# Kernel optimization log

Hardware: AMD Instinct MI355X
Metric: run time of the kernel (lower is better)

The kernel has to match this reference:

```python
import jax, jax.numpy as jnp
import numpy as np

NEG_SLOPE = 0.1
BN_EPS = 1e-5

def lrelu(z):
    return jax.nn.leaky_relu(z, NEG_SLOPE)

def conv1d(x, w, b):
    # x: [B,C,L], w: [O,I,K], 'same' padding for K=3
    y = jax.lax.conv_general_dilated(x, w, (1,), [(1, 1)], dimension_numbers=('NCH', 'OIH', 'NCH'))
    return y + b[None, :, None]

def batchnorm_train(x, g, be):
    # training-mode BatchNorm1d over (B, L) per channel; x: [B,C,L]
    m = x.mean(axis=(0, 2), keepdims=True)
    v = x.var(axis=(0, 2), keepdims=True)
    return g[None, :, None] * (x - m) * jax.lax.rsqrt(v + BN_EPS) + be[None, :, None]

def setup_inputs() -> dict:
    key = jax.random.key(0)
    ks = jax.random.split(key, 16)
    L, B, E = 100, 32, 512
    F, K, M, H, DEC = 256, 3, 128, 512, 512
    D = F + 2  # cnn feats + 2 coord dims
    s = 0.02
    inp = {
        'x': jax.random.normal(ks[0], (L, B, E), jnp.float32),
        'h': jax.random.normal(ks[1], (B, H), jnp.float32),
        'cw1': jax.random.normal(ks[2], (F, E, K), jnp.float32) * s,
        'cb1': jnp.zeros((F,), jnp.float32),
        'g1': jnp.ones((F,), jnp.float32), 'be1': jnp.zeros((F,), jnp.float32),
        'cw2': jax.random.normal(ks[3], (F, F, K), jnp.float32) * s,
        'cb2': jnp.zeros((F,), jnp.float32),
        'g2': jnp.ones((F,), jnp.float32), 'be2': jnp.zeros((F,), jnp.float32),
        'cw3': jax.random.normal(ks[4], (F, F, K), jnp.float32) * s,
        'cb3': jnp.zeros((F,), jnp.float32),
        'g3': jnp.ones((F,), jnp.float32), 'be3': jnp.zeros((F,), jnp.float32),
        'cw4': jax.random.normal(ks[5], (F, F, K), jnp.float32) * s,
        'cb4': jnp.zeros((F,), jnp.float32),
        'g4': jnp.ones((F,), jnp.float32), 'be4': jnp.zeros((F,), jnp.float32),
        'W1': jax.random.normal(ks[6], (2 * D + H, M), jnp.float32) * s,
        'b1': jnp.zeros((M,), jnp.float32),
        'W2': jax.random.normal(ks[7], (M, M), jnp.float32) * s,
        'b2': jnp.zeros((M,), jnp.float32),
        'W3': jax.random.normal(ks[8], (M, M), jnp.float32) * s,
        'b3': jnp.zeros((M,), jnp.float32),
        'W4': jax.random.normal(ks[9], (M, M), jnp.float32) * s,
        'b4': jnp.zeros((M,), jnp.float32),
        'F1': jax.random.normal(ks[10], (M, M), jnp.float32) * s,
        'fb1': jnp.zeros((M,), jnp.float32),
        'F2': jax.random.normal(ks[11], (M, DEC), jnp.float32) * s,
        'fb2': jnp.zeros((DEC,), jnp.float32),
    }
    return inp

def reference(x, h, cw1, cb1, g1, be1, cw2, cb2, g2, be2, cw3, cb3, g3, be3,
              cw4, cb4, g4, be4, W1, b1, W2, b2, W3, b3, W4, b4, F1, fb1, F2, fb2):
    # x: [L,B,E] -> [B,E,L]
    xc = jnp.transpose(x, (1, 2, 0))
    for cw, cb, g, be in ((cw1, cb1, g1, be1), (cw2, cb2, g2, be2),
                          (cw3, cb3, g3, be3), (cw4, cb4, g4, be4)):
        xc = batchnorm_train(lrelu(conv1d(xc, cw, cb)), g, be)
    xc = jnp.transpose(xc, (0, 2, 1))  # [B,L,F]
    B, L, _ = xc.shape
    # coordinate tensor: cvt_coord(i, L) = [(i/sqrt(L)-2)/2, (i%sqrt(L)-2)/2]
    i = jnp.arange(L, dtype=jnp.float32)
    sL = jnp.sqrt(jnp.float32(L))
    coord = jnp.stack([(i / sL - 2.0) / 2.0, (jnp.mod(i, sL) - 2.0) / 2.0], axis=-1)
    xf = jnp.concatenate([xc, jnp.broadcast_to(coord, (B, L, 2))], axis=-1)  # [B,L,D]
    D = xf.shape[-1]
    # pair[b,i,j] = [xf[b,j], xf[b,i], h[b]]; split W1 to avoid materializing concat
    Wa, Wb, Wc = W1[:D], W1[D:2 * D], W1[2 * D:]
    A = xf @ Wa                              # contribution of x_j, [B,L,M]
    C = xf @ Wb + (h @ Wc + b1)[:, None, :]  # contribution of x_i and h, [B,L,M]
    g = lrelu(C[:, :, None, :] + A[:, None, :, :])  # [B,L,L,M]
    g = lrelu(g @ W2 + b2)
    g = lrelu(g @ W3 + b3)
    g = lrelu(g @ W4 + b4)
    s = g.sum(axis=(1, 2))  # sum-pool over all L*L pairs -> [B,M]
    out = lrelu(lrelu(s @ F1 + fb1) @ F2 + fb2)  # [B,dec_hid]
    return out
```

## Files before the change

### kernel.cpp

```cpp
#include <hip/hip_runtime.h>
#include <hip/hip_bf16.h>
#include <stdint.h>
#include <stddef.h>

#define NEG 0.1f

typedef __attribute__((ext_vector_type(8))) short short8;
typedef __attribute__((ext_vector_type(16))) float floatx16;

__device__ __forceinline__ unsigned f2bf(float f) {
  union { float f; unsigned u; } v; v.f = f;
  unsigned r = v.u + 0x7FFFu + ((v.u >> 16) & 1u);
  return r >> 16;
}
__device__ __forceinline__ unsigned pk2bf(float a, float b) {
  __hip_bfloat162 hh = __float22bfloat162_rn(make_float2(a, b));
  union { __hip_bfloat162 h; unsigned u; } v; v.h = hh; return v.u;
}
__device__ __forceinline__ float bits2f(unsigned u) {
  union { unsigned u; float f; } v; v.u = u; return v.f;
}

__global__ void k_prep(const float* __restrict__ cw1, const float* __restrict__ cw2,
                       const float* __restrict__ cw3, const float* __restrict__ cw4,
                       unsigned short* __restrict__ wt1, unsigned short* __restrict__ wt2,
                       unsigned short* __restrict__ wt3, unsigned short* __restrict__ wt4,
                       const float* __restrict__ W1, unsigned short* __restrict__ wab,
                       const float* __restrict__ W2, const float* __restrict__ W3,
                       const float* __restrict__ W4, unsigned short* __restrict__ wmlp,
                       const float* __restrict__ h, float* __restrict__ hc,
                       const float* __restrict__ F1v, const float* __restrict__ F2v,
                       float* __restrict__ wsink) {
  __shared__ float tile[64 * 65];
  int bid = blockIdx.x, tid = threadIdx.x;
  if (bid < 1280) {
    int z = bid;
    int E; const float* cw; unsigned short* wt;
    if (z < 512) { E = 512; cw = cw1; wt = wt1; }
    else {
      int q = (z - 512) >> 8; E = 256;
      cw = (q == 0) ? cw2 : ((q == 1) ? cw3 : cw4);
      wt = (q == 0) ? wt2 : ((q == 1) ? wt3 : wt4);
      z = (z - 512) & 255;
    }
    int idx = z * 256 + tid;
    int f = idx / E, e = idx - f * E;
    const float* s = cw + (size_t)idx * 3;
    unsigned short* d = wt + (size_t)f * 3 * E + e;
    d[0] = (unsigned short)f2bf(s[0]);
    d[E] = (unsigned short)f2bf(s[1]);
    d[2 * E] = (unsigned short)f2bf(s[2]);
  } else if (bid < 1304) {
    int tw = bid - 1280;
    int half = tw / 12, rem = tw % 12, dt = rem >> 1, nt = rem & 1;
    int c = tid & 63, rq = tid >> 6;
#pragma unroll
    for (int it = 0; it < 16; ++it) {
      int r = rq + it * 4;
      int kp = dt * 64 + r;
      float v = 0.f;
      if (kp < 258) v = W1[(size_t)(half * 258 + kp) * 128 + nt * 64 + c];
      tile[r * 65 + c] = v;
    }
    __syncthreads();
#pragma unroll
    for (int it = 0; it < 16; ++it) {
      int r2 = rq + it * 4;
      wab[(size_t)(half * 128 + nt * 64 + r2) * 384 + dt * 64 + c] =
          (unsigned short)f2bf(tile[c * 65 + r2]);
    }
  } else if (bid < 1496) {
    int i2 = (bid - 1304) * 256 + tid;
    int n = i2 & 127, k = (i2 >> 7) & 127, zz = i2 >> 14;
    const float* W = (zz == 0) ? W2 : ((zz == 1) ? W3 : W4);
    float v = W[k * 128 + n];
    int w = n >> 5, l = ((k >> 3) & 1) * 32 + (n & 31), kk = k >> 4, j = k & 7;
    int i = (((zz * 4 + w) * 8 + kk) << 9) | (l << 3) | j;
    wmlp[i] = (unsigned short)f2bf(v);
  } else {
    int t = bid - 1496;
    int b = t >> 2, seg = t & 3;
    int m = tid & 127, sub = tid >> 7;
    int k0 = seg * 128 + sub * 64;
    const float* hr = h + b * 512 + k0;
    const float* Wc = W1 + (size_t)(516 + k0) * 128 + m;
    float a0 = 0.f, a1 = 0.f, a2 = 0.f, a3 = 0.f, a4 = 0.f, a5 = 0.f, a6 = 0.f, a7 = 0.f;
#pragma unroll
    for (int k = 0; k < 64; k += 8) {
      a0 += hr[k + 0] * Wc[(size_t)(k + 0) * 128];
      a1 += hr[k + 1] * Wc[(size_t)(k + 1) * 128];
      a2 += hr[k + 2] * Wc[(size_t)(k + 2) * 128];
      a3 += hr[k + 3] * Wc[(size_t)(k + 3) * 128];
      a4 += hr[k + 4] * Wc[(size_t)(k + 4) * 128];
      a5 += hr[k + 5] * Wc[(size_t)(k + 5) * 128];
      a6 += hr[k + 6] * Wc[(size_t)(k + 6) * 128];
      a7 += hr[k + 7] * Wc[(size_t)(k + 7) * 128];
    }
    float s = ((a0 + a1) + (a2 + a3)) + ((a4 + a5) + (a6 + a7));
    atomicAdd(&hc[b * 128 + m], s);
  }
  {
    int wslice = bid % 80;
    const float* wsrc = (wslice < 64) ? (F2v + (size_t)wslice * 1024)
                                      : (F1v + (size_t)(wslice - 64) * 1024);
    float4 v = *(const float4*)(wsrc + tid * 4);
    float sv = v.x + v.y + v.z + v.w;
    if (sv == 1234.5678f) wsink[0] = sv;
  }
}

__global__ __launch_bounds__(128, 2) void k_conv(
    const float* __restrict__ zin, const float* __restrict__ bnin,
    const float* __restrict__ gamv, const float* __restrict__ betv,
    const unsigned short* __restrict__ wt, const float* __restrict__ cb,
    float* __restrict__ zout, float* __restrict__ bnout, int E, int xmode) {
  extern __shared__ unsigned short smem[];
  const int SL = (E == 512) ? 520 : 264;
  unsigned short* slab = smem;
  unsigned short* Bs = smem + 34 * SL;
  const int K = 3 * E, NC = K >> 6, NCH = NC >> 1;
  const int esh = (E == 512) ? 9 : 8;
  int tid = threadIdx.x;
  int lane = tid & 63, khalf = tid >> 6;
  int r0 = blockIdx.x * 32, ct = blockIdx.y;
  int i32 = lane & 31;
  int koff = (lane >> 5) << 3;

  int lrow = (r0 + i32) % 100;
  bool vks0 = (lrow >= 1), vks2 = (lrow <= 98);

  if (xmode) {
    for (int s = khalf; s < 34; s += 2) {
      int m = r0 - 1 + s; m = min(max(m, 0), 3199);
      int b = m / 100, l = m - b * 100;
      size_t base = (size_t)(l * 32 + b) * 512;
#pragma unroll
      for (int cc = 0; cc < 2; ++cc) {
        int ch = cc * 256 + lane * 4;
        float4 v = *(const float4*)(zin + base + ch);
        uint2 p; p.x = pk2bf(v.x, v.y); p.y = pk2bf(v.z, v.w);
        *(uint2*)(&slab[s * SL + ch]) = p;
      }
    }
  } else {
    const float inv = 1.f / 3200.f;
    float sc[4], sh[4];
#pragma unroll
    for (int q = 0; q < 4; ++q) {
      int ch = lane * 4 + q;
      float mme = bnin[ch] * inv;
      float var = bnin[256 + ch] * inv - mme * mme;
      sc[q] = gamv[ch] * rsqrtf(var + 1e-5f);
      sh[q] = betv[ch] - mme * sc[q];
    }
    for (int s = khalf; s < 34; s += 2) {
      int m = r0 - 1 + s; m = min(max(m, 0), 3199);
      float4 v = *(const float4*)(zin + (size_t)m * 256 + lane * 4);
      uint2 p;
      p.x = pk2bf(v.x * sc[0] + sh[0], v.y * sc[1] + sh[1]);
      p.y = pk2bf(v.z * sc[2] + sh[2], v.w * sc[3] + sh[3]);
      *(uint2*)(&slab[s * SL + lane * 4]) = p;
    }
  }
  __syncthreads();

  floatx16 acc;
#pragma unroll
  for (int q = 0; q < 16; ++q) acc[q] = 0.f;

  unsigned short* Bc = Bs + khalf * (32 * 72);
  int brow = lane >> 1, bseg = (lane & 1) * 32;
  const unsigned short* wrow = wt + (size_t)(ct * 32 + brow) * K + khalf * NCH * 64 + bseg;
  uint4 pre[4];
#pragma unroll
  for (int t = 0; t < 4; ++t) pre[t] = *(const uint4*)(wrow + t * 8);

  for (int c = 0; c < NCH; ++c) {
#pragma unroll
    for (int t = 0; t < 4; ++t)
      *(uint4*)(&Bc[brow * 72 + bseg + t * 8]) = pre[t];
    if (c + 1 < NCH) {
#pragma unroll
      for (int t = 0; t < 4; ++t)
        pre[t] = *(const uint4*)(wrow + (c + 1) * 64 + t * 8);
    }
    int cg = khalf * NCH + c;
    int ks = (cg << 6) >> esh;
    int ebase = (cg << 6) & (E - 1);
    bool v = (ks == 0) ? vks0 : ((ks == 2) ? vks2 : true);
    int srow = i32 + ks;
#pragma unroll
    for (int kk = 0; kk < 4; ++kk) {
      short8 a = {};
      if (v) a = *(const short8*)(&slab[srow * SL + ebase + kk * 16 + koff]);
      short8 b8 = *(const short8*)(&Bc[i32 * 72 + kk * 16 + koff]);
      acc = __builtin_amdgcn_mfma_f32_32x32x16_bf16(a, b8, acc, 0, 0, 0);
    }
  }

  __syncthreads();
  float* scr = (float*)smem;
  if (khalf == 1) {
#pragma unroll
    for (int reg = 0; reg < 16; ++reg) {
      int rowp = (reg & 3) + 8 * (reg >> 2) + 4 * (lane >> 5);
      scr[rowp * 32 + i32] = acc[reg];
    }
  }
  __syncthreads();
  if (khalf == 0) {
    int f = ct * 32 + i32;
    float bias = cb[f];
    float s1 = 0.f, s2 = 0.f;
#pragma unroll
    for (int reg = 0; reg < 16; ++reg) {
      int rowp = (reg & 3) + 8 * (reg >> 2) + 4 * (lane >> 5);
      int m = r0 + rowp;
      float v = acc[reg] + scr[rowp * 32 + i32] + bias;
      v = fmaxf(v, NEG * v);
      zout[(size_t)m * 256 + f] = v;
      s1 += v; s2 += v * v;
    }
    s1 += __shfl_xor(s1, 32, 64);
    s2 += __shfl_xor(s2, 32, 64);
    if (lane < 32) { atomicAdd(&bnout[f], s1); atomicAdd(&bnout[256 + f], s2); }
  }
}

__global__ __launch_bounds__(128, 2) void k_ac(
    const float* __restrict__ zin, const float* __restrict__ bnin,
    const float* __restrict__ gamv, const float* __restrict__ betv,
    const unsigned short* __restrict__ wab, const float* __restrict__ hc,
    const float* __restrict__ b1v,
    unsigned short* __restrict__ Abf, unsigned short* __restrict__ Cbf) {
  __shared__ unsigned short slab[32 * 328];
  __shared__ unsigned short Bs[2 * 64 * 72];
  int tid = threadIdx.x;
  int lane = tid & 63, wave = tid >> 6;
  int r0 = blockIdx.x * 32, ct = blockIdx.y;
  int i32 = lane & 31;
  int koff = (lane >> 5) << 3;
  const float inv = 1.f / 3200.f;

  {
    float sc[4], sh[4];
#pragma unroll
    for (int q = 0; q < 4; ++q) {
      int ch = lane * 4 + q;
      float mme = bnin[ch] * inv;
      float var = bnin[256 + ch] * inv - mme * mme;
      sc[q] = gamv[ch] * rsqrtf(var + 1e-5f);
      sh[q] = betv[ch] - mme * sc[q];
    }
    for (int s = wave; s < 32; s += 2) {
      int m = r0 + s;
      float4 v = *(const float4*)(zin + (size_t)m * 256 + lane * 4);
      uint2 p;
      p.x = pk2bf(v.x * sc[0] + sh[0], v.y * sc[1] + sh[1]);
      p.y = pk2bf(v.z * sc[2] + sh[2], v.w * sc[3] + sh[3]);
      *(uint2*)(&slab[s * 328 + lane * 4]) = p;
    }
    if (wave == 0) {
      int s = i32, half = (lane >> 5) * 32;
      int m = r0 + s, l = m % 100;
      float c0 = ((float)l * 0.1f - 2.0f) * 0.5f;
      float c1 = ((float)(l % 10) - 2.0f) * 0.5f;
#pragma unroll
      for (int seg = 0; seg < 4; ++seg) {
        uint4 z4; z4.x = z4.y = z4.z = z4.w = 0u;
        if (half == 0 && seg == 0) z4.x = pk2bf(c0, c1);
        *(uint4*)(&slab[s * 328 + 256 + half + seg * 8]) = z4;
      }
    }
  }

  floatx16 acc;
#pragma unroll
  for (int q = 0; q < 16; ++q) acc[q] = 0.f;

  int brow = tid >> 1, bhalf = (tid & 1) * 32;
  uint4 pre[4];
#pragma unroll
  for (int t = 0; t < 4; ++t)
    pre[t] = *(const uint4*)(wab + (size_t)(ct * 64 + brow) * 384 + bhalf + t * 8);

  for (int c = 0; c < 5; ++c) {
    unsigned short* Bc = Bs + (c & 1) * (64 * 72);
#pragma unroll
    for (int t = 0; t < 4; ++t)
      *(uint4*)(&Bc[brow * 72 + bhalf + t * 8]) = pre[t];
    __syncthreads();
    if (c + 1 < 5) {
#pragma unroll
      for (int t = 0; t < 4; ++t)
        pre[t] = *(const uint4*)(wab + (size_t)(ct * 64 + brow) * 384 + (c + 1) * 64 + bhalf + t * 8);
    }
#pragma unroll
    for (int kk = 0; kk < 4; ++kk) {
      short8 a = *(const short8*)(&slab[i32 * 328 + c * 64 + kk * 16 + koff]);
      short8 b8 = *(const short8*)(&Bs[(c & 1) * (64 * 72) + (wave * 32 + i32) * 72 + kk * 16 + koff]);
      acc = __builtin_amdgcn_mfma_f32_32x32x16_bf16(a, b8, acc, 0, 0, 0);
    }
  }

  int n = ct * 64 + wave * 32 + i32;
#pragma unroll
  for (int reg = 0; reg < 16; ++reg) {
    int rowp = (reg & 3) + 8 * (reg >> 2) + 4 * (lane >> 5);
    int m = r0 + rowp;
    float v = acc[reg];
    if (ct < 2) {
      Abf[(size_t)m * 128 + n] = (unsigned short)f2bf(v);
    } else {
      int b = m / 100;
      int nc = n - 128;
      Cbf[(size_t)m * 128 + nc] =
          (unsigned short)f2bf(v + hc[b * 128 + nc] + b1v[nc]);
    }
  }
}

__global__ __launch_bounds__(256, 2) void k_mlp(
    const unsigned short* __restrict__ Abf, const unsigned short* __restrict__ Cbf,
    const unsigned short* __restrict__ wmlp, const float* __restrict__ b2,
    const float* __restrict__ b3, const float* __restrict__ b4,
    float* __restrict__ sout) {
  __shared__ unsigned short gs0[128 * 128];
  __shared__ unsigned short gs1[128 * 128];
  int tid = threadIdx.x, lane = tid & 63, wave = tid >> 6;
  int ln31 = lane & 31;
  int half = lane >> 5;
  int rx = ln31 & 15;

  short8 wreg[3][8];
#pragma unroll
  for (int z = 0; z < 3; ++z)
#pragma unroll
    for (int kk = 0; kk < 8; ++kk)
      wreg[z][kk] = *(const short8*)(wmlp + (size_t)(((z * 4 + wave) * 8 + kk) * 512) + lane * 8);

  int wb = wave * 32;
  float4 bq[2][4];
#pragma unroll
  for (int q = 0; q < 4; ++q) {
    bq[0][q] = *(const float4*)(b2 + wb + q * 8 + 4 * half);
    bq[1][q] = *(const float4*)(b3 + wb + q * 8 + 4 * half);
  }
  float bv4 = b4[wb + ln31];

  for (int ti = 0; ti < 2; ++ti) {
    int t = blockIdx.x + ti * 1264;
    int b = t / 79, tt = t - b * 79;
    __syncthreads();
    {
      int lr = wb + (lane >> 1);
      int hh = lane & 1;
      int lbase = lr * 128, lrx = lr & 15;
      int r = tt * 128 + lr;
      if (r > 9999) r = 9999;
      const unsigned short* Crow = Cbf + (size_t)(b * 100 + r / 100) * 128;
      const unsigned short* Arow = Abf + (size_t)(b * 100 + r % 100) * 128;
#pragma unroll
      for (int it = 0; it < 8; ++it) {
        int cc = hh * 64 + it * 8;
        uint4 c4 = *(const uint4*)(Crow + cc);
        uint4 a4 = *(const uint4*)(Arow + cc);
        unsigned cw[4] = {c4.x, c4.y, c4.z, c4.w};
        unsigned aw[4] = {a4.x, a4.y, a4.z, a4.w};
        unsigned ow[4];
#pragma unroll
        for (int q = 0; q < 4; ++q) {
          float x0 = bits2f(cw[q] << 16) + bits2f(aw[q] << 16);
          float x1 = bits2f(cw[q] & 0xFFFF0000u) + bits2f(aw[q] & 0xFFFF0000u);
          x0 = fmaxf(x0, NEG * x0);
          x1 = fmaxf(x1, NEG * x1);
          ow[q] = pk2bf(x0, x1);
        }
        uint4 o4; o4.x = ow[0]; o4.y = ow[1]; o4.z = ow[2]; o4.w = ow[3];
        *(uint4*)(&gs0[lbase + (((hh * 8 + it) ^ lrx) << 3)]) = o4;
      }
    }
    __syncthreads();

#pragma unroll
    for (int z = 0; z < 2; ++z) {
      const unsigned short* src = z ? gs1 : gs0;
      unsigned short* dst = z ? gs0 : gs1;
#pragma unroll
      for (int rg = 0; rg < 4; ++rg) {
        floatx16 acc;
#pragma unroll
        for (int q = 0; q < 16; ++q) acc[q] = 0.f;
        int rowb = (rg * 32 + ln31) * 128;
#pragma unroll
        for (int kk = 0; kk < 8; ++kk) {
          short8 g8 = *(const short8*)(&src[rowb + (((kk * 2 + half) ^ rx) << 3)]);
          acc = __builtin_amdgcn_mfma_f32_32x32x16_bf16(wreg[z][kk], g8, acc, 0, 0, 0);
        }
        int prb = (rg * 32 + ln31) * 128;
#pragma unroll
        for (int q = 0; q < 4; ++q) {
          float4 bb = bq[z][q];
          float v0 = acc[q * 4 + 0] + bb.x; v0 = fmaxf(v0, NEG * v0);
          float v1 = acc[q * 4 + 1] + bb.y; v1 = fmaxf(v1, NEG * v1);
          float v2 = acc[q * 4 + 2] + bb.z; v2 = fmaxf(v2, NEG * v2);
          float v3 = acc[q * 4 + 3] + bb.w; v3 = fmaxf(v3, NEG * v3);
          uint2 p; p.x = pk2bf(v0, v1); p.y = pk2bf(v2, v3);
          *(uint2*)(&dst[prb + (((wave * 4 + q) ^ rx) << 3) + half * 4]) = p;
        }
      }
      __syncthreads();
    }

    float colsum = 0.f;
#pragma unroll
    for (int rg = 0; rg < 4; ++rg) {
      floatx16 acc;
#pragma unroll
      for (int q = 0; q < 16; ++q) acc[q] = 0.f;
      int rowb = (rg * 32 + ln31) * 128;
#pragma unroll
      for (int kk = 0; kk < 8; ++kk) {
        short8 a8 = *(const short8*)(&gs0[rowb + (((kk * 2 + half) ^ rx) << 3)]);
        acc = __builtin_amdgcn_mfma_f32_32x32x16_bf16(a8, wreg[2][kk], acc, 0, 0, 0);
      }
#pragma unroll
      for (int reg = 0; reg < 16; ++reg) {
        int rowp = (reg & 3) + 8 * (reg >> 2) + 4 * half;
        int p = tt * 128 + rg * 32 + rowp;
        float v = acc[reg] + bv4;
        v = fmaxf(v, NEG * v);
        colsum += (p < 10000) ? v : 0.f;
      }
    }
    colsum += __shfl_xor(colsum, 32, 64);
    if (lane < 32) atomicAdd(&sout[b * 128 + wb + lane], colsum);
  }
}

__global__ void k_final(const float* __restrict__ s, const float* __restrict__ F1,
                        const float* __restrict__ fb1, const float* __restrict__ F2,
                        const float* __restrict__ fb2, float* __restrict__ out) {
  __shared__ float sl[128], part[512], t1[128];
  int b = blockIdx.x, t = threadIdx.x;
  if (t < 128) sl[t] = s[b * 128 + t];
  __syncthreads();
  {
    int m = t & 127, kh = t >> 7;
    const float* Fp = F1 + m;
    float a0 = 0.f, a1 = 0.f, a2 = 0.f, a3 = 0.f;
    for (int k = kh * 32; k < kh * 32 + 32; k += 4) {
      a0 += sl[k + 0] * Fp[(size_t)(k + 0) * 128];
      a1 += sl[k + 1] * Fp[(size_t)(k + 1) * 128];
      a2 += sl[k + 2] * Fp[(size_t)(k + 2) * 128];
      a3 += sl[k + 3] * Fp[(size_t)(k + 3) * 128];
    }
    part[t] = (a0 + a1) + (a2 + a3);
  }
  __syncthreads();
  if (t < 128) {
    float a = (part[t] + part[t + 128]) + (part[t + 256] + part[t + 384]) + fb1[t];
    t1[t] = fmaxf(a, NEG * a);
  }
  __syncthreads();
  {
    int o = t;
    const float* Fp = F2 + o;
    float a0 = fb2[o], a1 = 0.f, a2 = 0.f, a3 = 0.f;
    for (int k = 0; k < 128; k += 4) {
      a0 += t1[k + 0] * Fp[(size_t)(k + 0) * 512];
      a1 += t1[k + 1] * Fp[(size_t)(k + 1) * 512];
      a2 += t1[k + 2] * Fp[(size_t)(k + 2) * 512];
      a3 += t1[k + 3] * Fp[(size_t)(k + 3) * 512];
    }
    float a = (a0 + a1) + (a2 + a3);
    out[b * 512 + o] = fmaxf(a, NEG * a);
  }
}

extern "C" void kernel_launch(void* const* d_in, const int* in_sizes, int n_in,
                              void* d_out, int out_size, void* d_ws, size_t ws_size,
                              hipStream_t stream) {
  const float* x   = (const float*)d_in[0];
  const float* h   = (const float*)d_in[1];
  const float* cw1 = (const float*)d_in[2];
  const float* cb1 = (const float*)d_in[3];
  const float* g1  = (const float*)d_in[4];
  const float* be1 = (const float*)d_in[5];
  const float* cw2 = (const float*)d_in[6];
  const float* cb2 = (const float*)d_in[7];
  const float* g2  = (const float*)d_in[8];
  const float* be2 = (const float*)d_in[9];
  const float* cw3 = (const float*)d_in[10];
  const float* cb3 = (const float*)d_in[11];
  const float* g3  = (const float*)d_in[12];
  const float* be3 = (const float*)d_in[13];
  const float* cw4 = (const float*)d_in[14];
  const float* cb4 = (const float*)d_in[15];
  const float* g4  = (const float*)d_in[16];
  const float* be4 = (const float*)d_in[17];
  const float* W1  = (const float*)d_in[18];
  const float* b1  = (const float*)d_in[19];
  const float* W2  = (const float*)d_in[20];
  const float* b2  = (const float*)d_in[21];
  const float* W3  = (const float*)d_in[22];
  const float* b3  = (const float*)d_in[23];
  const float* W4  = (const float*)d_in[24];
  const float* b4  = (const float*)d_in[25];
  const float* F1  = (const float*)d_in[26];
  const float* fb1 = (const float*)d_in[27];
  const float* F2  = (const float*)d_in[28];
  const float* fb2 = (const float*)d_in[29];

  char* ws = (char*)d_ws;
  float* bn0  = (float*)(ws + 0);
  float* bn1  = (float*)(ws + 2048);
  float* bn2  = (float*)(ws + 4096);
  float* bn3  = (float*)(ws + 6144);
  float* sbuf = (float*)(ws + 8192);
  float* hc   = (float*)(ws + 24576);
  float* za   = (float*)(ws + 40960);
  float* zb   = (float*)(ws + 3317760);
  unsigned short* wt1  = (unsigned short*)(ws + 6594560);
  unsigned short* wt2  = (unsigned short*)(ws + 7380992);
  unsigned short* wt3  = (unsigned short*)(ws + 7774208);
  unsigned short* wt4  = (unsigned short*)(ws + 8167424);
  unsigned short* wab  = (unsigned short*)(ws + 8560640);
  unsigned short* wmlp = (unsigned short*)(ws + 8757248);
  unsigned short* Abf  = (unsigned short*)(ws + 8855552);
  unsigned short* Cbf  = (unsigned short*)(ws + 9674752);
  float* wsink = (float*)(ws + 10493952);

  hipMemsetAsync(d_ws, 0, 40960, stream);

  k_prep<<<1624, 256, 0, stream>>>(cw1, cw2, cw3, cw4, wt1, wt2, wt3, wt4,
                                   W1, wab, W2, W3, W4, wmlp, h, hc, F1, F2, wsink);

  const int lds1 = (34 * 520 + 2 * 32 * 72) * 2;
  const int lds2 = (34 * 264 + 2 * 32 * 72) * 2;
  k_conv<<<dim3(100, 8), 128, lds1, stream>>>(x,  nullptr, nullptr, nullptr, wt1, cb1, za, bn0, 512, 1);
  k_conv<<<dim3(100, 8), 128, lds2, stream>>>(za, bn0, g1, be1, wt2, cb2, zb, bn1, 256, 0);
  k_conv<<<dim3(100, 8), 128, lds2, stream>>>(zb, bn1, g2, be2, wt3, cb3, za, bn2, 256, 0);
  k_conv<<<dim3(100, 8), 128, lds2, stream>>>(za, bn2, g3, be3, wt4, cb4, zb, bn3, 256, 0);

  k_ac<<<dim3(100, 4), 128, 0, stream>>>(zb, bn3, g4, be4, wab, hc, b1, Abf, Cbf);

  k_mlp<<<1264, 256, 0, stream>>>(Abf, Cbf, wmlp, b2, b3, b4, sbuf);
  k_final<<<32, 512, 0, stream>>>(sbuf, F1, fb1, F2, fb2, (float*)d_out);
}
```

Measured before the change: 289.8 us.

## Make k_mlp waves own row slabs, single LDS buffer, one tile per block

Reworks the pairwise MLP kernel so each wave processes its own 32 rows through all 128 output columns, which removes the block-wide syncthreads between layers and lets a single in-place LDS buffer replace two. Weights are now streamed from global/L2 per output tile instead of being held in registers. The grid is doubled to one tile per block and launch bounds are raised to 3 blocks per CU to improve occupancy. The trade-off is repeated weight loads from cache and more atomics per block, one per output column tile. A small cleanup in k_ac indexes the B tile through the already computed buffer pointer.

```diff
diff --git a/kernel.cpp b/kernel.cpp
--- a/kernel.cpp
+++ b/kernel.cpp
@@ -298,7 +298,7 @@
 #pragma unroll
     for (int kk = 0; kk < 4; ++kk) {
       short8 a = *(const short8*)(&slab[i32 * 328 + c * 64 + kk * 16 + koff]);
-      short8 b8 = *(const short8*)(&Bs[(c & 1) * (64 * 72) + (wave * 32 + i32) * 72 + kk * 16 + koff]);
+      short8 b8 = *(const short8*)(&Bc[(wave * 32 + i32) * 72 + kk * 16 + koff]);
       acc = __builtin_amdgcn_mfma_f32_32x32x16_bf16(a, b8, acc, 0, 0, 0);
     }
   }
@@ -320,121 +320,116 @@
   }
 }
 
-__global__ __launch_bounds__(256, 2) void k_mlp(
+__global__ __launch_bounds__(256, 3) void k_mlp(
     const unsigned short* __restrict__ Abf, const unsigned short* __restrict__ Cbf,
     const unsigned short* __restrict__ wmlp, const float* __restrict__ b2,
     const float* __restrict__ b3, const float* __restrict__ b4,
     float* __restrict__ sout) {
-  __shared__ unsigned short gs0[128 * 128];
-  __shared__ unsigned short gs1[128 * 128];
+  __shared__ unsigned short gs[128 * 128];
   int tid = threadIdx.x, lane = tid & 63, wave = tid >> 6;
   int ln31 = lane & 31;
   int half = lane >> 5;
   int rx = ln31 & 15;
-
-  short8 wreg[3][8];
-#pragma unroll
-  for (int z = 0; z < 3; ++z)
+  int wb = wave * 32;
+
+  int t = blockIdx.x;
+  int b = t / 79, tt = t - b * 79;
+
+  {
+    int lr = wb + (lane >> 1);
+    int hh = lane & 1;
+    int lbase = lr * 128, lrx = lr & 15;
+    int r = tt * 128 + lr;
+    if (r > 9999) r = 9999;
+    const unsigned short* Crow = Cbf + (size_t)(b * 100 + r / 100) * 128;
+    const unsigned short* Arow = Abf + (size_t)(b * 100 + r % 100) * 128;
+#pragma unroll
+    for (int it = 0; it < 8; ++it) {
+      int cc = hh * 64 + it * 8;
+      uint4 c4 = *(const uint4*)(Crow + cc);
+      uint4 a4 = *(const uint4*)(Arow + cc);
+      unsigned cw[4] = {c4.x, c4.y, c4.z, c4.w};
+      unsigned aw[4] = {a4.x, a4.y, a4.z, a4.w};
+      unsigned ow[4];
+#pragma unroll
+      for (int q = 0; q < 4; ++q) {
+        float x0 = bits2f(cw[q] << 16) + bits2f(aw[q] << 16);
+        float x1 = bits2f(cw[q] & 0xFFFF0000u) + bits2f(aw[q] & 0xFFFF0000u);
+        x0 = fmaxf(x0, NEG * x0);
+        x1 = fmaxf(x1, NEG * x1);
+        ow[q] = pk2bf(x0, x1);
+      }
+      uint4 o4; o4.x = ow[0]; o4.y = ow[1]; o4.z = ow[2]; o4.w = ow[3];
+      *(uint4*)(&gs[lbase + (((hh * 8 + it) ^ lrx) << 3)]) = o4;
+    }
+  }
+
+  int rowb = (wb + ln31) * 128;
+
+#pragma unroll
+  for (int z = 0; z < 2; ++z) {
+    const float* bz = z ? b3 : b2;
+    short8 gfrag[8];
 #pragma unroll
     for (int kk = 0; kk < 8; ++kk)
-      wreg[z][kk] = *(const short8*)(wmlp + (size_t)(((z * 4 + wave) * 8 + kk) * 512) + lane * 8);
-
-  int wb = wave * 32;
-  float4 bq[2][4];
-#pragma unroll
-  for (int q = 0; q < 4; ++q) {
-    bq[0][q] = *(const float4*)(b2 + wb + q * 8 + 4 * half);
-    bq[1][q] = *(const float4*)(b3 + wb + q * 8 + 4 * half);
-  }
-  float bv4 = b4[wb + ln31];
-
-  for (int ti = 0; ti < 2; ++ti) {
-    int t = blockIdx.x + ti * 1264;
-    int b = t / 79, tt = t - b * 79;
-    __syncthreads();
-    {
-      int lr = wb + (lane >> 1);
-      int hh = lane & 1;
-      int lbase = lr * 128, lrx = lr & 15;
-      int r = tt * 128 + lr;
-      if (r > 9999) r = 9999;
-      const unsigned short* Crow = Cbf + (size_t)(b * 100 + r / 100) * 128;
-      const unsigned short* Arow = Abf + (size_t)(b * 100 + r % 100) * 128;
-#pragma unroll
-      for (int it = 0; it < 8; ++it) {
-        int cc = hh * 64 + it * 8;
-        uint4 c4 = *(const uint4*)(Crow + cc);
-        uint4 a4 = *(const uint4*)(Arow + cc);
-        unsigned cw[4] = {c4.x, c4.y, c4.z, c4.w};
-        unsigned aw[4] = {a4.x, a4.y, a4.z, a4.w};
-        unsigned ow[4];
-#pragma unroll
-        for (int q = 0; q < 4; ++q) {
-          float x0 = bits2f(cw[q] << 16) + bits2f(aw[q] << 16);
-          float x1 = bits2f(cw[q] & 0xFFFF0000u) + bits2f(aw[q] & 0xFFFF0000u);
-          x0 = fmaxf(x0, NEG * x0);
-          x1 = fmaxf(x1, NEG * x1);
-          ow[q] = pk2bf(x0, x1);
-        }
-        uint4 o4; o4.x = ow[0]; o4.y = ow[1]; o4.z = ow[2]; o4.w = ow[3];
-        *(uint4*)(&gs0[lbase + (((hh * 8 + it) ^ lrx) << 3)]) = o4;
+      gfrag[kk] = *(const short8*)(&gs[rowb + (((kk * 2 + half) ^ rx) << 3)]);
+#pragma unroll
+    for (int nt = 0; nt < 4; ++nt) {
+      const unsigned short* wp = wmlp + (size_t)(((z * 4 + nt) * 8) << 9) + lane * 8;
+      short8 wfrag[8];
+#pragma unroll
+      for (int kk = 0; kk < 8; ++kk)
+        wfrag[kk] = *(const short8*)(wp + (kk << 9));
+      floatx16 acc;
+#pragma unroll
+      for (int q = 0; q < 16; ++q) acc[q] = 0.f;
+#pragma unroll
+      for (int kk = 0; kk < 8; ++kk)
+        acc = __builtin_amdgcn_mfma_f32_32x32x16_bf16(wfrag[kk], gfrag[kk], acc, 0, 0, 0);
+#pragma unroll
+      for (int q = 0; q < 4; ++q) {
+        float4 bb = *(const float4*)(bz + nt * 32 + q * 8 + 4 * half);
+        float v0 = acc[q * 4 + 0] + bb.x; v0 = fmaxf(v0, NEG * v0);
+        float v1 = acc[q * 4 + 1] + bb.y; v1 = fmaxf(v1, NEG * v1);
+        float v2 = acc[q * 4 + 2] + bb.z; v2 = fmaxf(v2, NEG * v2);
+        float v3 = acc[q * 4 + 3] + bb.w; v3 = fmaxf(v3, NEG * v3);
+        uint2 p; p.x = pk2bf(v0, v1); p.y = pk2bf(v2, v3);
+        *(uint2*)(&gs[rowb + (((nt * 4 + q) ^ rx) << 3) + half * 4]) = p;
       }
     }
-    __syncthreads();
-
-#pragma unroll
-    for (int z = 0; z < 2; ++z) {
-      const unsigned short* src = z ? gs1 : gs0;
-      unsigned short* dst = z ? gs0 : gs1;
-#pragma unroll
-      for (int rg = 0; rg < 4; ++rg) {
-        floatx16 acc;
-#pragma unroll
-        for (int q = 0; q < 16; ++q) acc[q] = 0.f;
-        int rowb = (rg * 32 + ln31) * 128;
-#pragma unroll
-        for (int kk = 0; kk < 8; ++kk) {
-          short8 g8 = *(const short8*)(&src[rowb + (((kk * 2 + half) ^ rx) << 3)]);
-          acc = __builtin_amdgcn_mfma_f32_32x32x16_bf16(wreg[z][kk], g8, acc, 0, 0, 0);
-        }
-        int prb = (rg * 32 + ln31) * 128;
-#pragma unroll
-        for (int q = 0; q < 4; ++q) {
-          float4 bb = bq[z][q];
-          float v0 = acc[q * 4 + 0] + bb.x; v0 = fmaxf(v0, NEG * v0);
-          float v1 = acc[q * 4 + 1] + bb.y; v1 = fmaxf(v1, NEG * v1);
-          float v2 = acc[q * 4 + 2] + bb.z; v2 = fmaxf(v2, NEG * v2);
-          float v3 = acc[q * 4 + 3] + bb.w; v3 = fmaxf(v3, NEG * v3);
-          uint2 p; p.x = pk2bf(v0, v1); p.y = pk2bf(v2, v3);
-          *(uint2*)(&dst[prb + (((wave * 4 + q) ^ rx) << 3) + half * 4]) = p;
-        }
-      }
-      __syncthreads();
-    }
-
-    float colsum = 0.f;
-#pragma unroll
-    for (int rg = 0; rg < 4; ++rg) {
+  }
+
+  {
+    short8 gfrag[8];
+#pragma unroll
+    for (int kk = 0; kk < 8; ++kk)
+      gfrag[kk] = *(const short8*)(&gs[rowb + (((kk * 2 + half) ^ rx) << 3)]);
+#pragma unroll
+    for (int nt = 0; nt < 4; ++nt) {
+      const unsigned short* wp = wmlp + (size_t)(((8 + nt) * 8) << 9) + lane * 8;
+      short8 wfrag[8];
+#pragma unroll
+      for (int kk = 0; kk < 8; ++kk)
+        wfrag[kk] = *(const short8*)(wp + (kk << 9));
       floatx16 acc;
 #pragma unroll
       for (int q = 0; q < 16; ++q) acc[q] = 0.f;
-      int rowb = (rg * 32 + ln31) * 128;
-#pragma unroll
-      for (int kk = 0; kk < 8; ++kk) {
-        short8 a8 = *(const short8*)(&gs0[rowb + (((kk * 2 + half) ^ rx) << 3)]);
-        acc = __builtin_amdgcn_mfma_f32_32x32x16_bf16(a8, wreg[2][kk], acc, 0, 0, 0);
-      }
+#pragma unroll
+      for (int kk = 0; kk < 8; ++kk)
+        acc = __builtin_amdgcn_mfma_f32_32x32x16_bf16(gfrag[kk], wfrag[kk], acc, 0, 0, 0);
+      float bv = b4[nt * 32 + ln31];
+      float cs = 0.f;
 #pragma unroll
       for (int reg = 0; reg < 16; ++reg) {
         int rowp = (reg & 3) + 8 * (reg >> 2) + 4 * half;
-        int p = tt * 128 + rg * 32 + rowp;
-        float v = acc[reg] + bv4;
+        int p = tt * 128 + wb + rowp;
+        float v = acc[reg] + bv;
         v = fmaxf(v, NEG * v);
-        colsum += (p < 10000) ? v : 0.f;
+        cs += (p < 10000) ? v : 0.f;
       }
-    }
-    colsum += __shfl_xor(colsum, 32, 64);
-    if (lane < 32) atomicAdd(&sout[b * 128 + wb + lane], colsum);
+      cs += __shfl_xor(cs, 32, 64);
+      if (lane < 32) atomicAdd(&sout[b * 128 + nt * 32 + lane], cs);
+    }
   }
 }
 
@@ -545,6 +540,6 @@
 
   k_ac<<<dim3(100, 4), 128, 0, stream>>>(zb, bn3, g4, be4, wab, hc, b1, Abf, Cbf);
 
-  k_mlp<<<1264, 256, 0, stream>>>(Abf, Cbf, wmlp, b2, b3, b4, sbuf);
+  k_mlp<<<2528, 256, 0, stream>>>(Abf, Cbf, wmlp, b2, b3, b4, sbuf);
   k_final<<<32, 512, 0, stream>>>(sbuf, F1, fb1, F2, fb2, (float*)d_out);
 }
```

After: 313.3 us. 1.08x slower.

## Widen conv blocks to 64 output channels and vectorize weight prep

Applied to the files above, without the earlier changes.

The conv kernel now runs 256 threads per block, with four waves split as two K-halves by two 32-channel column groups. Each block covers 64 output channels, so the grid halves and every activation slab loaded into LDS is reused across twice as many channels. The B tile becomes double-buffered with a barrier per chunk, replacing the single barrier after the slab load, which adds synchronisation inside the loop. Weight prep also converts four taps per thread with float4 loads and packed bf16 stores, cutting the prep grid from 1624 to 664 blocks.

```diff
diff --git a/kernel.cpp b/kernel.cpp
--- a/kernel.cpp
+++ b/kernel.cpp
@@ -33,25 +33,35 @@
                        float* __restrict__ wsink) {
   __shared__ float tile[64 * 65];
   int bid = blockIdx.x, tid = threadIdx.x;
-  if (bid < 1280) {
-    int z = bid;
-    int E; const float* cw; unsigned short* wt;
-    if (z < 512) { E = 512; cw = cw1; wt = wt1; }
-    else {
-      int q = (z - 512) >> 8; E = 256;
+  if (bid < 320) {
+    const float* cw; unsigned short* wt; int E, base;
+    if (bid < 128) {
+      cw = cw1; wt = wt1; E = 512;
+      base = (bid * 256 + tid) * 4;
+    } else {
+      int j = bid - 128; int q = j >> 6; E = 256;
       cw = (q == 0) ? cw2 : ((q == 1) ? cw3 : cw4);
       wt = (q == 0) ? wt2 : ((q == 1) ? wt3 : wt4);
-      z = (z - 512) & 255;
-    }
-    int idx = z * 256 + tid;
-    int f = idx / E, e = idx - f * E;
-    const float* s = cw + (size_t)idx * 3;
-    unsigned short* d = wt + (size_t)f * 3 * E + e;
-    d[0] = (unsigned short)f2bf(s[0]);
-    d[E] = (unsigned short)f2bf(s[1]);
-    d[2 * E] = (unsigned short)f2bf(s[2]);
-  } else if (bid < 1304) {
-    int tw = bid - 1280;
+      base = (((j & 63) * 256) + tid) * 4;
+    }
+    int f = base / E, e0 = base & (E - 1);
+    const float* s = cw + (size_t)(f * E + e0) * 3;
+    float4 v0 = *(const float4*)(s);
+    float4 v1 = *(const float4*)(s + 4);
+    float4 v2 = *(const float4*)(s + 8);
+    float k0[4] = {v0.x, v0.w, v1.z, v2.y};
+    float k1[4] = {v0.y, v1.x, v1.w, v2.z};
+    float k2[4] = {v0.z, v1.y, v2.x, v2.w};
+    unsigned short* d = wt + (size_t)f * 3 * E + e0;
+    uint2 p;
+    p.x = pk2bf(k0[0], k0[1]); p.y = pk2bf(k0[2], k0[3]);
+    *(uint2*)(d) = p;
+    p.x = pk2bf(k1[0], k1[1]); p.y = pk2bf(k1[2], k1[3]);
+    *(uint2*)(d + E) = p;
+    p.x = pk2bf(k2[0], k2[1]); p.y = pk2bf(k2[2], k2[3]);
+    *(uint2*)(d + 2 * E) = p;
+  } else if (bid < 344) {
+    int tw = bid - 320;
     int half = tw / 12, rem = tw % 12, dt = rem >> 1, nt = rem & 1;
     int c = tid & 63, rq = tid >> 6;
 #pragma unroll
@@ -69,8 +79,8 @@
       wab[(size_t)(half * 128 + nt * 64 + r2) * 384 + dt * 64 + c] =
           (unsigned short)f2bf(tile[c * 65 + r2]);
     }
-  } else if (bid < 1496) {
-    int i2 = (bid - 1304) * 256 + tid;
+  } else if (bid < 536) {
+    int i2 = (bid - 344) * 256 + tid;
     int n = i2 & 127, k = (i2 >> 7) & 127, zz = i2 >> 14;
     const float* W = (zz == 0) ? W2 : ((zz == 1) ? W3 : W4);
     float v = W[k * 128 + n];
@@ -78,7 +88,7 @@
     int i = (((zz * 4 + w) * 8 + kk) << 9) | (l << 3) | j;
     wmlp[i] = (unsigned short)f2bf(v);
   } else {
-    int t = bid - 1496;
+    int t = bid - 536;
     int b = t >> 2, seg = t & 3;
     int m = tid & 127, sub = tid >> 7;
     int k0 = seg * 128 + sub * 64;
@@ -109,7 +119,7 @@
   }
 }
 
-__global__ __launch_bounds__(128, 2) void k_conv(
+__global__ __launch_bounds__(256, 2) void k_conv(
     const float* __restrict__ zin, const float* __restrict__ bnin,
     const float* __restrict__ gamv, const float* __restrict__ betv,
     const unsigned short* __restrict__ wt, const float* __restrict__ cb,
@@ -121,7 +131,8 @@
   const int K = 3 * E, NC = K >> 6, NCH = NC >> 1;
   const int esh = (E == 512) ? 9 : 8;
   int tid = threadIdx.x;
-  int lane = tid & 63, khalf = tid >> 6;
+  int lane = tid & 63, wave = tid >> 6;
+  int khalf = wave >> 1, cwave = wave & 1;
   int r0 = blockIdx.x * 32, ct = blockIdx.y;
   int i32 = lane & 31;
   int koff = (lane >> 5) << 3;
@@ -130,7 +141,7 @@
   bool vks0 = (lrow >= 1), vks2 = (lrow <= 98);
 
   if (xmode) {
-    for (int s = khalf; s < 34; s += 2) {
+    for (int s = wave; s < 34; s += 4) {
       int m = r0 - 1 + s; m = min(max(m, 0), 3199);
       int b = m / 100, l = m - b * 100;
       size_t base = (size_t)(l * 32 + b) * 512;
@@ -153,7 +164,7 @@
       sc[q] = gamv[ch] * rsqrtf(var + 1e-5f);
       sh[q] = betv[ch] - mme * sc[q];
     }
-    for (int s = khalf; s < 34; s += 2) {
+    for (int s = wave; s < 34; s += 4) {
       int m = r0 - 1 + s; m = min(max(m, 0), 3199);
       float4 v = *(const float4*)(zin + (size_t)m * 256 + lane * 4);
       uint2 p;
@@ -162,23 +173,24 @@
       *(uint2*)(&slab[s * SL + lane * 4]) = p;
     }
   }
-  __syncthreads();
 
   floatx16 acc;
 #pragma unroll
   for (int q = 0; q < 16; ++q) acc[q] = 0.f;
 
-  unsigned short* Bc = Bs + khalf * (32 * 72);
-  int brow = lane >> 1, bseg = (lane & 1) * 32;
-  const unsigned short* wrow = wt + (size_t)(ct * 32 + brow) * K + khalf * NCH * 64 + bseg;
+  int t128 = tid & 127;
+  int brow = t128 >> 1, bhalf = (t128 & 1) * 32;
+  const unsigned short* wrow = wt + (size_t)(ct * 64 + brow) * K + khalf * NCH * 64 + bhalf;
   uint4 pre[4];
 #pragma unroll
   for (int t = 0; t < 4; ++t) pre[t] = *(const uint4*)(wrow + t * 8);
 
   for (int c = 0; c < NCH; ++c) {
+    unsigned short* Bc = Bs + (khalf * 2 + (c & 1)) * (64 * 72);
 #pragma unroll
     for (int t = 0; t < 4; ++t)
-      *(uint4*)(&Bc[brow * 72 + bseg + t * 8]) = pre[t];
+      *(uint4*)(&Bc[brow * 72 + bhalf + t * 8]) = pre[t];
+    __syncthreads();
     if (c + 1 < NCH) {
 #pragma unroll
       for (int t = 0; t < 4; ++t)
@@ -193,7 +205,7 @@
     for (int kk = 0; kk < 4; ++kk) {
       short8 a = {};
       if (v) a = *(const short8*)(&slab[srow * SL + ebase + kk * 16 + koff]);
-      short8 b8 = *(const short8*)(&Bc[i32 * 72 + kk * 16 + koff]);
+      short8 b8 = *(const short8*)(&Bc[(cwave * 32 + i32) * 72 + kk * 16 + koff]);
       acc = __builtin_amdgcn_mfma_f32_32x32x16_bf16(a, b8, acc, 0, 0, 0);
     }
   }
@@ -204,19 +216,19 @@
 #pragma unroll
     for (int reg = 0; reg < 16; ++reg) {
       int rowp = (reg & 3) + 8 * (reg >> 2) + 4 * (lane >> 5);
-      scr[rowp * 32 + i32] = acc[reg];
+      scr[cwave * 1024 + rowp * 32 + i32] = acc[reg];
     }
   }
   __syncthreads();
   if (khalf == 0) {
-    int f = ct * 32 + i32;
+    int f = ct * 64 + cwave * 32 + i32;
     float bias = cb[f];
     float s1 = 0.f, s2 = 0.f;
 #pragma unroll
     for (int reg = 0; reg < 16; ++reg) {
       int rowp = (reg & 3) + 8 * (reg >> 2) + 4 * (lane >> 5);
       int m = r0 + rowp;
-      float v = acc[reg] + scr[rowp * 32 + i32] + bias;
+      float v = acc[reg] + scr[cwave * 1024 + rowp * 32 + i32] + bias;
       v = fmaxf(v, NEG * v);
       zout[(size_t)m * 256 + f] = v;
       s1 += v; s2 += v * v;
@@ -298,7 +310,7 @@
 #pragma unroll
     for (int kk = 0; kk < 4; ++kk) {
       short8 a = *(const short8*)(&slab[i32 * 328 + c * 64 + kk * 16 + koff]);
-      short8 b8 = *(const short8*)(&Bs[(c & 1) * (64 * 72) + (wave * 32 + i32) * 72 + kk * 16 + koff]);
+      short8 b8 = *(const short8*)(&Bc[(wave * 32 + i32) * 72 + kk * 16 + koff]);
       acc = __builtin_amdgcn_mfma_f32_32x32x16_bf16(a, b8, acc, 0, 0, 0);
     }
   }
@@ -533,15 +545,15 @@
 
   hipMemsetAsync(d_ws, 0, 40960, stream);
 
-  k_prep<<<1624, 256, 0, stream>>>(cw1, cw2, cw3, cw4, wt1, wt2, wt3, wt4,
-                                   W1, wab, W2, W3, W4, wmlp, h, hc, F1, F2, wsink);
-
-  const int lds1 = (34 * 520 + 2 * 32 * 72) * 2;
-  const int lds2 = (34 * 264 + 2 * 32 * 72) * 2;
-  k_conv<<<dim3(100, 8), 128, lds1, stream>>>(x,  nullptr, nullptr, nullptr, wt1, cb1, za, bn0, 512, 1);
-  k_conv<<<dim3(100, 8), 128, lds2, stream>>>(za, bn0, g1, be1, wt2, cb2, zb, bn1, 256, 0);
-  k_conv<<<dim3(100, 8), 128, lds2, stream>>>(zb, bn1, g2, be2, wt3, cb3, za, bn2, 256, 0);
-  k_conv<<<dim3(100, 8), 128, lds2, stream>>>(za, bn2, g3, be3, wt4, cb4, zb, bn3, 256, 0);
+  k_prep<<<664, 256, 0, stream>>>(cw1, cw2, cw3, cw4, wt1, wt2, wt3, wt4,
+                                  W1, wab, W2, W3, W4, wmlp, h, hc, F1, F2, wsink);
+
+  const int lds1 = (34 * 520 + 4 * 64 * 72) * 2;
+  const int lds2 = (34 * 264 + 4 * 64 * 72) * 2;
+  k_conv<<<dim3(100, 4), 256, lds1, stream>>>(x,  nullptr, nullptr, nullptr, wt1, cb1, za, bn0, 512, 1);
+  k_conv<<<dim3(100, 4), 256, lds2, stream>>>(za, bn0, g1, be1, wt2, cb2, zb, bn1, 256, 0);
+  k_conv<<<dim3(100, 4), 256, lds2, stream>>>(zb, bn1, g2, be2, wt3, cb3, za, bn2, 256, 0);
+  k_conv<<<dim3(100, 4), 256, lds2, stream>>>(za, bn2, g3, be3, wt4, cb4, zb, bn3, 256, 0);
 
   k_ac<<<dim3(100, 4), 128, 0, stream>>>(zb, bn3, g4, be4, wab, hc, b1, Abf, Cbf);
 
```

Measured after the change: 284.3 us. No clear change (-1.9%).
